# Kernel tuning notes

Hardware: AMD Instinct MI355X
Metric: run time of the kernel (lower is better)

## Reference

```python
import jax, jax.numpy as jnp
import numpy as np

BS, D, NC, N, C, K = 8192, 1024, 64, 100000, 1000, 50


def setup_inputs() -> dict:
    key = jax.random.key(0)
    k1, k2, k3, k4, k5 = jax.random.split(key, 5)
    return {
        "train_embedding": jax.random.normal(k1, (BS, D), dtype=jnp.float32),
        # concept initialized uniform in [-0.5, 0.5] as in init_concept
        "concept": jax.random.uniform(k2, (D, NC), dtype=jnp.float32, minval=-0.5, maxval=0.5),
        "bank": jax.random.normal(k3, (N, D), dtype=jnp.float32),
        "W_h": jax.random.normal(k4, (D, C), dtype=jnp.float32) * 0.02,
        "b_h": jax.random.normal(k5, (C,), dtype=jnp.float32) * 0.02,
        "topk": K,
    }


def reference(train_embedding, concept, bank, W_h, b_h, topk):
    # h_x: linear classifier head
    def h_x(z):
        return z @ W_h + b_h

    # projection onto concept subspace: C (C^T C)^{-1} C^T
    G = concept.T @ concept                      # [nc, nc]
    proj_matrix = concept @ jnp.linalg.inv(G) @ concept.T  # [D, D]
    proj = train_embedding @ proj_matrix.T       # (proj_matrix @ X^T)^T -> [bs, D]
    y_pred = h_x(proj)                           # [bs, C]
    orig_pred = h_x(train_embedding)             # [bs, C]

    # batched per-concept Euclidean distance to the whole bank: [nc, N]
    bank_sq = jnp.sum(bank * bank, axis=1)       # [N]
    con_sq = jnp.sum(concept * concept, axis=0)  # [nc]
    d2 = con_sq[:, None] - 2.0 * (concept.T @ bank.T) + bank_sq[None, :]
    dist = jnp.sqrt(jnp.maximum(d2, 0.0))
    # topk SMALLEST distances per concept
    _, idx = jax.lax.top_k(-dist, topk)          # idx: [nc, k]
    knn = bank[idx]                              # [nc, k, D] gather

    # L_sparse_1: mean over concepts of (c . mean_k knn)
    dots = jnp.einsum('dn,nkd->n', concept, knn) / topk  # [nc]
    L_sparse_1 = jnp.mean(dots)

    nc = concept.shape[1]
    eye = jnp.eye(nc, dtype=concept.dtype)
    L_sparse_2 = jnp.mean(G * (1.0 - eye))       # off-diagonal mean
    norm_metrics = jnp.mean(G * eye)             # diagonal mean

    return (orig_pred, y_pred, L_sparse_1, L_sparse_2, norm_metrics)
```

## Files before the change

kernel.cpp:

```cpp
#include <hip/hip_runtime.h>
#include <cstddef>

#define BSZ   8192
#define DIM   1024
#define NCON  64
#define NBANK 100000
#define NCLS  1000
#define TOPK  50
#define NCHUNK 32
#define CHUNK  3125
#define CHUNKP 3328
#define NDIST 1563

#define Y_OFF 8192000
#define S_OFF 16384000

typedef __attribute__((ext_vector_type(8))) short bf16x8;
typedef __attribute__((ext_vector_type(4))) float f32x4;

__device__ __forceinline__ short f2bf(float x) {
    unsigned u = __builtin_bit_cast(unsigned, x);
    unsigned r = (u + 0x7fffu + ((u >> 16) & 1u)) >> 16;
    return (short)r;
}

__device__ __forceinline__ bf16x8 pack8(f32x4 a, f32x4 b) {
    bf16x8 p;
    p[0] = f2bf(a[0]); p[1] = f2bf(a[1]); p[2] = f2bf(a[2]); p[3] = f2bf(a[3]);
    p[4] = f2bf(b[0]); p[5] = f2bf(b[1]); p[6] = f2bf(b[2]); p[7] = f2bf(b[3]);
    return p;
}

__device__ __forceinline__ void gload16(const void* g, void* l) {
    __builtin_amdgcn_global_load_lds(
        (__attribute__((address_space(1))) void*)g,
        (__attribute__((address_space(3))) void*)l,
        16, 0, 0);
}

__global__ void __launch_bounds__(256) prep_kernel(const float* __restrict__ cpt,
                                                   const float* __restrict__ Wh,
                                                   short* __restrict__ WhT,
                                                   short* __restrict__ cptT) {
    __shared__ short Ts[64][65];
    int b = blockIdx.x;
    int t = threadIdx.x;
    if (b < 256) {
        int k0 = (b & 15) * 64, n0 = (b >> 4) * 64;
        #pragma unroll
        for (int i = 0; i < 16; ++i) {
            int u = i * 256 + t;
            int kL = u >> 6, nL = u & 63;
            int n = n0 + nL;
            Ts[kL][nL] = (n < NCLS) ? f2bf(Wh[(size_t)(k0 + kL) * NCLS + n]) : (short)0;
        }
        __syncthreads();
        #pragma unroll
        for (int i = 0; i < 16; ++i) {
            int u = i * 256 + t;
            int nL = u >> 6, kL = u & 63;
            WhT[(size_t)(n0 + nL) * DIM + k0 + kL] = Ts[kL][nL];
        }
    } else {
        int q = b - 256;
        #pragma unroll
        for (int i = 0; i < 16; ++i) {
            int u = q * 4096 + i * 256 + t;
            int d = u >> 6, n = u & 63;
            cptT[n * DIM + d] = f2bf(cpt[u]);
        }
    }
}

__global__ void __launch_bounds__(256) mid_kernel(const float* __restrict__ bank,
                                                  const float* __restrict__ X,
                                                  const short* __restrict__ cptT,
                                                  const short* __restrict__ WhT,
                                                  short* __restrict__ Xbf,
                                                  short* __restrict__ XCbf,
                                                  float* __restrict__ key,
                                                  float* __restrict__ bank_sq,
                                                  short* __restrict__ MbfT,
                                                  float* __restrict__ G,
                                                  short* __restrict__ invGbf) {
    __shared__ __align__(16) char smem[49152];
    int b = blockIdx.x;
    int t = threadIdx.x;
    int wid = t >> 6, l = t & 63, lr = l & 15, lg = l >> 4;
    if (b < 8) {
        int c0 = b * 128;
        f32x4 acc[4][2] = {};
        for (int kk = 0; kk < DIM; kk += 32) {
            bf16x8 af[4], bfr[2];
            #pragma unroll
            for (int mi = 0; mi < 4; ++mi)
                af[mi] = *(const bf16x8*)(cptT + (mi * 16 + lr) * DIM + kk + lg * 8);
            #pragma unroll
            for (int ni = 0; ni < 2; ++ni)
                bfr[ni] = *(const bf16x8*)(WhT + (size_t)(c0 + wid * 32 + ni * 16 + lr) * DIM + kk + lg * 8);
            #pragma unroll
            for (int mi = 0; mi < 4; ++mi)
                #pragma unroll
                for (int ni = 0; ni < 2; ++ni)
                    acc[mi][ni] = __builtin_amdgcn_mfma_f32_16x16x32_bf16(af[mi], bfr[ni], acc[mi][ni], 0, 0, 0);
        }
        #pragma unroll
        for (int mi = 0; mi < 4; ++mi)
            #pragma unroll
            for (int ni = 0; ni < 2; ++ni)
                #pragma unroll
                for (int r = 0; r < 4; ++r) {
                    int m = mi * 16 + lg * 4 + r;
                    int c = c0 + wid * 32 + ni * 16 + lr;
                    MbfT[(size_t)c * NCON + m] = f2bf(acc[mi][ni][r]);
                }
    } else if (b == 8) {
        float* rowk = (float*)smem;
        float* fk = (float*)(smem + 256);
        f32x4 acc[4] = {};
        for (int kk = 0; kk < DIM; kk += 32) {
            bf16x8 af[4], bfr;
            #pragma unroll
            for (int mi = 0; mi < 4; ++mi)
                af[mi] = *(const bf16x8*)(cptT + (mi * 16 + lr) * DIM + kk + lg * 8);
            bfr = *(const bf16x8*)(cptT + (wid * 16 + lr) * DIM + kk + lg * 8);
            #pragma unroll
            for (int mi = 0; mi < 4; ++mi)
                acc[mi] = __builtin_amdgcn_mfma_f32_16x16x32_bf16(af[mi], bfr, acc[mi], 0, 0, 0);
        }
        #pragma unroll
        for (int mi = 0; mi < 4; ++mi)
            #pragma unroll
            for (int r = 0; r < 4; ++r)
                G[(mi * 16 + lg * 4 + r) * 64 + wid * 16 + lr] = acc[mi][r];
        __syncthreads();
        float myA[16];
        #pragma unroll
        for (int s = 0; s < 16; ++s) myA[s] = G[(4 * s + wid) * 64 + l];
        #pragma unroll
        for (int k = 0; k < 64; ++k) {
            if (wid == (k & 3)) rowk[l] = myA[k >> 2];
            if (l == k) {
                #pragma unroll
                for (int s = 0; s < 16; ++s) fk[4 * s + wid] = myA[s];
            }
            __syncthreads();
            float ip = 1.f / rowk[k];
            float rv = rowk[l];
            #pragma unroll
            for (int s = 0; s < 16; ++s) {
                int i = 4 * s + wid;
                float fv = fk[i];
                float nv;
                if (i == k && l == k)      nv = ip;
                else if (i == k)           nv = rv * ip;
                else if (l == k)           nv = -fv * ip;
                else                       nv = myA[s] - fv * (rv * ip);
                myA[s] = nv;
            }
            __syncthreads();
        }
        #pragma unroll
        for (int s = 0; s < 16; ++s) invGbf[(4 * s + wid) * 64 + l] = f2bf(myA[s]);
    } else if (b < 73) {
        int r0 = (b - 9) * 128;
        int r_[2];
        const float* xrow[2];
        #pragma unroll
        for (int ni = 0; ni < 2; ++ni) {
            r_[ni] = r0 + wid * 32 + ni * 16 + lr;
            xrow[ni] = X + (size_t)r_[ni] * DIM + lg * 8;
        }
        f32x4 acc[4][2] = {};
        for (int kk = 0; kk < DIM; kk += 32) {
            bf16x8 af[4];
            #pragma unroll
            for (int mi = 0; mi < 4; ++mi)
                af[mi] = *(const bf16x8*)(cptT + (mi * 16 + lr) * DIM + kk + lg * 8);
            #pragma unroll
            for (int ni = 0; ni < 2; ++ni) {
                f32x4 a = *(const f32x4*)(xrow[ni] + kk);
                f32x4 c = *(const f32x4*)(xrow[ni] + kk + 4);
                bf16x8 pk = pack8(a, c);
                *(bf16x8*)(Xbf + (size_t)r_[ni] * DIM + kk + lg * 8) = pk;
                #pragma unroll
                for (int mi = 0; mi < 4; ++mi)
                    acc[mi][ni] = __builtin_amdgcn_mfma_f32_16x16x32_bf16(af[mi], pk, acc[mi][ni], 0, 0, 0);
            }
        }
        #pragma unroll
        for (int mi = 0; mi < 4; ++mi)
            #pragma unroll
            for (int ni = 0; ni < 2; ++ni)
                #pragma unroll
                for (int r = 0; r < 4; ++r) {
                    int m = mi * 16 + lg * 4 + r;
                    XCbf[(size_t)r_[ni] * NCON + m] = f2bf(acc[mi][ni][r]);
                }
    } else {
        int j0 = (b - 73) * 64;
        int bj4[4], bs4[4];
        #pragma unroll
        for (int i = 0; i < 4; ++i) {
            int flat = i * 4096 + wid * 1024 + l * 16;
            bj4[i] = flat >> 8;
            bs4[i] = ((flat >> 4) & 15) ^ (bj4[i] & 15);
        }
        int cm2[2], cs2[2];
        #pragma unroll
        for (int i = 0; i < 2; ++i) {
            int flat = i * 4096 + wid * 1024 + l * 16;
            cm2[i] = flat >> 7;
            cs2[i] = ((flat >> 4) & 7) ^ (cm2[i] & 7);
        }
        int jl = wid * 16 + lr;
        f32x4 acc[4] = {};
        float sq = 0.f;
        #pragma unroll
        for (int i = 0; i < 4; ++i) {
            int jr = j0 + bj4[i]; if (jr >= NBANK) jr = NBANK - 1;
            gload16(bank + (size_t)jr * DIM + bs4[i] * 4, smem + i * 4096 + wid * 1024);
        }
        #pragma unroll
        for (int i = 0; i < 2; ++i)
            gload16(cptT + cm2[i] * DIM + cs2[i] * 8, smem + 32768 + i * 4096 + wid * 1024);
        int buf = 0;
        for (int kk = 0; kk < DIM; kk += 64) {
            __syncthreads();
            int kn = kk + 64;
            int nb = buf ^ 1;
            if (kn < DIM) {
                #pragma unroll
                for (int i = 0; i < 4; ++i) {
                    int jr = j0 + bj4[i]; if (jr >= NBANK) jr = NBANK - 1;
                    gload16(bank + (size_t)jr * DIM + kn + bs4[i] * 4,
                            smem + nb * 16384 + i * 4096 + wid * 1024);
                }
                #pragma unroll
                for (int i = 0; i < 2; ++i)
                    gload16(cptT + cm2[i] * DIM + kn + cs2[i] * 8,
                            smem + 32768 + nb * 8192 + i * 4096 + wid * 1024);
            }
            const float* bT = (const float*)(smem + buf * 16384);
            const short* cS = (const short*)(smem + 32768 + buf * 8192);
            #pragma unroll
            for (int ks = 0; ks < 2; ++ks) {
                bf16x8 af[4];
                #pragma unroll
                for (int mi = 0; mi < 4; ++mi) {
                    int m = mi * 16 + lr;
                    af[mi] = *(const bf16x8*)(cS + m * 64 + (((ks * 4 + lg) ^ (m & 7)) << 3));
                }
                int g0 = ks * 8 + lg * 2;
                f32x4 a = *(const f32x4*)(bT + jl * 64 + ((g0 ^ (jl & 15)) << 2));
                f32x4 c = *(const f32x4*)(bT + jl * 64 + (((g0 + 1) ^ (jl & 15)) << 2));
                sq += a[0]*a[0] + a[1]*a[1] + a[2]*a[2] + a[3]*a[3]
                    + c[0]*c[0] + c[1]*c[1] + c[2]*c[2] + c[3]*c[3];
                bf16x8 pk = pack8(a, c);
                #pragma unroll
                for (int mi = 0; mi < 4; ++mi)
                    acc[mi] = __builtin_amdgcn_mfma_f32_16x16x32_bf16(af[mi], pk, acc[mi], 0, 0, 0);
            }
            buf ^= 1;
        }
        sq += __shfl_xor(sq, 16);
        sq += __shfl_xor(sq, 32);
        int j = j0 + jl;
        if (j < NBANK) {
            if (lg == 0) bank_sq[j] = sq;
            #pragma unroll
            for (int mi = 0; mi < 4; ++mi)
                #pragma unroll
                for (int r = 0; r < 4; ++r) {
                    int m = mi * 16 + lg * 4 + r;
                    key[(size_t)m * NBANK + j] = sq - 2.f * acc[mi][r];
                }
        }
    }
}

__global__ void __launch_bounds__(256) topA_kernel(const float* __restrict__ key,
                                                   float* __restrict__ cand_v,
                                                   int* __restrict__ cand_j,
                                                   const short* __restrict__ invGbf,
                                                   const short* __restrict__ MbfT,
                                                   short* __restrict__ M2T) {
    __shared__ float vals[CHUNKP];
    __shared__ float wv[4];
    __shared__ int wj[4];
    int b = blockIdx.x;
    int t = threadIdx.x;
    if (b < 2048) {
        int n = b >> 5;
        int c = b & 31;
        int base = c * CHUNK;
        const float* row = key + (size_t)n * NBANK + base;
        float lv = __builtin_inff();
        int lj = 0x7fffffff;
        #pragma unroll 13
        for (int i = 0; i < 13; ++i) {
            int j = t + i * 256;
            float v = (j < CHUNK) ? row[j] : __builtin_inff();
            vals[j] = v;
            if (v < lv) { lv = v; lj = j; }
        }
        __syncthreads();
        float* cv = cand_v + (size_t)b * TOPK;
        int* cj = cand_j + (size_t)b * TOPK;
        for (int it = 0; it < TOPK; ++it) {
            float bv = lv; int bj = lj;
            #pragma unroll
            for (int o = 32; o > 0; o >>= 1) {
                float ov = __shfl_down(bv, o);
                int oj = __shfl_down(bj, o);
                if (ov < bv || (ov == bv && oj < bj)) { bv = ov; bj = oj; }
            }
            if ((t & 63) == 0) { wv[t >> 6] = bv; wj[t >> 6] = bj; }
            __syncthreads();
            float gv = wv[0]; int gj = wj[0];
            #pragma unroll
            for (int w2 = 1; w2 < 4; ++w2)
                if (wv[w2] < gv || (wv[w2] == gv && wj[w2] < gj)) { gv = wv[w2]; gj = wj[w2]; }
            if (t == 0) { cv[it] = gv; cj[it] = base + gj; }
            if (t == (gj & 255)) {
                vals[gj] = __builtin_inff();
                lv = __builtin_inff(); lj = 0x7fffffff;
                #pragma unroll 13
                for (int i = 0; i < 13; ++i) {
                    int j = t + i * 256;
                    float v = vals[j];
                    if (v < lv) { lv = v; lj = j; }
                }
            }
            __syncthreads();
        }
    } else {
        int c0 = (b - 2048) * 128;
        int wid = t >> 6, l = t & 63, lr = l & 15, lg = l >> 4;
        f32x4 acc[4][2] = {};
        #pragma unroll
        for (int ks = 0; ks < 2; ++ks) {
            bf16x8 af[4], bfr[2];
            #pragma unroll
            for (int mi = 0; mi < 4; ++mi)
                af[mi] = *(const bf16x8*)(invGbf + (mi * 16 + lr) * NCON + ks * 32 + lg * 8);
            #pragma unroll
            for (int ni = 0; ni < 2; ++ni)
                bfr[ni] = *(const bf16x8*)(MbfT + (size_t)(c0 + wid * 32 + ni * 16 + lr) * NCON + ks * 32 + lg * 8);
            #pragma unroll
            for (int mi = 0; mi < 4; ++mi)
                #pragma unroll
                for (int ni = 0; ni < 2; ++ni)
                    acc[mi][ni] = __builtin_amdgcn_mfma_f32_16x16x32_bf16(af[mi], bfr[ni], acc[mi][ni], 0, 0, 0);
        }
        #pragma unroll
        for (int mi = 0; mi < 4; ++mi)
            #pragma unroll
            for (int ni = 0; ni < 2; ++ni)
                #pragma unroll
                for (int r = 0; r < 4; ++r) {
                    int n = mi * 16 + lg * 4 + r;
                    int c = c0 + wid * 32 + ni * 16 + lr;
                    M2T[(size_t)c * NCON + n] = f2bf(acc[mi][ni][r]);
                }
    }
}

__global__ void __launch_bounds__(256) pred_kernel(const short* __restrict__ Xbf,
                                                   const short* __restrict__ WhT,
                                                   const short* __restrict__ XCbf,
                                                   const short* __restrict__ M2T,
                                                   const float* __restrict__ bh,
                                                   const float* __restrict__ cand_v,
                                                   const int* __restrict__ cand_j,
                                                   const float* __restrict__ bank_sq,
                                                   float* __restrict__ orig,
                                                   float* __restrict__ ypred,
                                                   float* __restrict__ dots) {
    __shared__ __align__(16) char smem[32768];
    int b = blockIdx.x;
    int t = threadIdx.x;
    int wid = t >> 6, l = t & 63, lr = l & 15, lg = l >> 4;
    if (b < 512) {
        short* As = (short*)smem;
        short* Bs = (short*)(smem + 16384);
        int c0 = (b & 7) * 128;
        int r0 = (b >> 3) * 128;
        int wr = wid >> 1, wc = wid & 1;
        int srow_off = l >> 3;
        int scol = ((l & 7) ^ (l >> 3)) * 8;
        f32x4 acc[4][4] = {};
        for (int kk = 0; kk < DIM; kk += 64) {
            if (kk) __syncthreads();
            #pragma unroll
            for (int i = 0; i < 4; ++i) {
                int si = wid * 4 + i;
                int row = si * 8 + srow_off;
                gload16(Xbf + (size_t)(r0 + row) * DIM + kk + scol, As + si * 512);
                gload16(WhT + (size_t)(c0 + row) * DIM + kk + scol, Bs + si * 512);
            }
            __syncthreads();
            #pragma unroll
            for (int ks = 0; ks < 2; ++ks) {
                bf16x8 af[4], bfr[4];
                #pragma unroll
                for (int mi = 0; mi < 4; ++mi) {
                    int rr = wr * 64 + mi * 16 + lr;
                    int slot = (ks * 4 + lg) ^ (rr & 7);
                    af[mi] = *(const bf16x8*)(As + rr * 64 + slot * 8);
                }
                #pragma unroll
                for (int ni = 0; ni < 4; ++ni) {
                    int cc = wc * 64 + ni * 16 + lr;
                    int slot = (ks * 4 + lg) ^ (cc & 7);
                    bfr[ni] = *(const bf16x8*)(Bs + cc * 64 + slot * 8);
                }
                #pragma unroll
                for (int mi = 0; mi < 4; ++mi)
                    #pragma unroll
                    for (int ni = 0; ni < 4; ++ni)
                        acc[mi][ni] = __builtin_amdgcn_mfma_f32_16x16x32_bf16(af[mi], bfr[ni], acc[mi][ni], 0, 0, 0);
            }
        }
        #pragma unroll
        for (int mi = 0; mi < 4; ++mi)
            #pragma unroll
            for (int ni = 0; ni < 4; ++ni) {
                int col = c0 + wc * 64 + ni * 16 + lr;
                if (col < NCLS) {
                    float bias = bh[col];
                    #pragma unroll
                    for (int r = 0; r < 4; ++r) {
                        int row = r0 + wr * 64 + mi * 16 + lg * 4 + r;
                        orig[(size_t)row * NCLS + col] = acc[mi][ni][r] + bias;
                    }
                }
            }
    } else if (b < 1024) {
        int q = b - 512;
        int c0 = (q & 7) * 128;
        int r0 = (q >> 3) * 128;
        int wr = wid >> 1, wc = wid & 1;
        f32x4 acc[4][4] = {};
        #pragma unroll
        for (int ks = 0; ks < 2; ++ks) {
            bf16x8 af[4], bfr[4];
            #pragma unroll
            for (int mi = 0; mi < 4; ++mi)
                af[mi] = *(const bf16x8*)(XCbf + (size_t)(r0 + wr * 64 + mi * 16 + lr) * NCON + ks * 32 + lg * 8);
            #pragma unroll
            for (int ni = 0; ni < 4; ++ni)
                bfr[ni] = *(const bf16x8*)(M2T + (size_t)(c0 + wc * 64 + ni * 16 + lr) * NCON + ks * 32 + lg * 8);
            #pragma unroll
            for (int mi = 0; mi < 4; ++mi)
                #pragma unroll
                for (int ni = 0; ni < 4; ++ni)
                    acc[mi][ni] = __builtin_amdgcn_mfma_f32_16x16x32_bf16(af[mi], bfr[ni], acc[mi][ni], 0, 0, 0);
        }
        #pragma unroll
        for (int mi = 0; mi < 4; ++mi)
            #pragma unroll
            for (int ni = 0; ni < 4; ++ni) {
                int col = c0 + wc * 64 + ni * 16 + lr;
                if (col < NCLS) {
                    float bias = bh[col];
                    #pragma unroll
                    for (int r = 0; r < 4; ++r) {
                        int row = r0 + wr * 64 + mi * 16 + lg * 4 + r;
                        ypred[(size_t)row * NCLS + col] = acc[mi][ni][r] + bias;
                    }
                }
            }
    } else {
        int n = b - 1024;
        const int NC2 = NCHUNK * TOPK;
        float* vals = (float*)smem;
        int* gidx = (int*)(smem + 6400);
        float* wv = (float*)(smem + 12800);
        int* wj = (int*)(smem + 12816);
        int* wl = (int*)(smem + 12832);
        for (int j = t; j < NC2; j += 256) {
            vals[j] = cand_v[(size_t)n * NC2 + j];
            gidx[j] = cand_j[(size_t)n * NC2 + j];
        }
        __syncthreads();
        float sum = 0.f;
        for (int it = 0; it < TOPK; ++it) {
            float bv = __builtin_inff();
            int bj = 0x7fffffff;
            int bl = -1;
            #pragma unroll 7
            for (int j = t; j < NC2; j += 256) {
                float v = vals[j];
                int gj = gidx[j];
                if (v < bv || (v == bv && gj < bj)) { bv = v; bj = gj; bl = j; }
            }
            #pragma unroll
            for (int o = 32; o > 0; o >>= 1) {
                float ov = __shfl_down(bv, o);
                int oj = __shfl_down(bj, o);
                int ol = __shfl_down(bl, o);
                if (ov < bv || (ov == bv && oj < bj)) { bv = ov; bj = oj; bl = ol; }
            }
            if ((t & 63) == 0) { wv[t >> 6] = bv; wj[t >> 6] = bj; wl[t >> 6] = bl; }
            __syncthreads();
            if (t == 0) {
                #pragma unroll
                for (int w2 = 1; w2 < 4; ++w2)
                    if (wv[w2] < bv || (wv[w2] == bv && wj[w2] < bj)) { bv = wv[w2]; bj = wj[w2]; bl = wl[w2]; }
                sum += 0.5f * (bank_sq[bj] - bv);
                vals[bl] = __builtin_inff();
            }
            __syncthreads();
        }
        if (t == 0) dots[n] = sum / (float)TOPK;
    }
}

__global__ void __launch_bounds__(256) fin_kernel(const float* __restrict__ G,
                                                  const float* __restrict__ dots,
                                                  float* __restrict__ out3) {
    __shared__ float r1[256], r2[256], r3[256];
    int t = threadIdx.x;
    float sd = 0.f, so = 0.f;
    for (int u = t; u < 4096; u += 256) {
        float g = G[u];
        if ((u >> 6) == (u & 63)) sd += g; else so += g;
    }
    float s1 = (t < NCON) ? dots[t] : 0.f;
    r1[t] = sd; r2[t] = so; r3[t] = s1;
    __syncthreads();
    for (int o = 128; o > 0; o >>= 1) {
        if (t < o) { r1[t] += r1[t + o]; r2[t] += r2[t + o]; r3[t] += r3[t + o]; }
        __syncthreads();
    }
    if (t == 0) {
        out3[0] = r3[0] / 64.f;
        out3[1] = r2[0] / 4096.f;
        out3[2] = r1[0] / 4096.f;
    }
}

extern "C" void kernel_launch(void* const* d_in, const int* in_sizes, int n_in,
                              void* d_out, int out_size, void* d_ws, size_t ws_size,
                              hipStream_t stream) {
    const float* X    = (const float*)d_in[0];
    const float* cpt  = (const float*)d_in[1];
    const float* bank = (const float*)d_in[2];
    const float* Wh   = (const float*)d_in[3];
    const float* bh   = (const float*)d_in[4];
    float* out = (float*)d_out;

    float* orig  = out;
    float* ypred = out + Y_OFF;
    float* out3  = out + S_OFF;

    char* w = (char*)d_ws;
    short* Xbf    = (short*)(w);
    short* WhT    = (short*)(w + 16777216);
    short* cptT   = (short*)(w + 18874368);
    short* XCbf   = (short*)(w + 19005440);
    short* M2T    = (short*)(w + 20054016);
    float* key    = (float*)(w + 20185088);
    float* bank_sq= (float*)(w + 45785088);
    float* G      = (float*)(w + 46185472);
    short* invGbf = (short*)(w + 46201856);
    short* MbfT   = (short*)(w + 46210048);
    float* cand_v = (float*)(w + 46341120);
    int*   cand_j = (int*)  (w + 46750720);
    float* dots   = (float*)(w + 47160320);

    prep_kernel<<<272, 256, 0, stream>>>(cpt, Wh, WhT, cptT);
    mid_kernel<<<73 + NDIST, 256, 0, stream>>>(bank, X, cptT, WhT, Xbf, XCbf, key, bank_sq, MbfT, G, invGbf);
    topA_kernel<<<2056, 256, 0, stream>>>(key, cand_v, cand_j, invGbf, MbfT, M2T);
    pred_kernel<<<1088, 256, 0, stream>>>(Xbf, WhT, XCbf, M2T, bh, cand_v, cand_j, bank_sq, orig, ypred, dots);
    fin_kernel<<<1, 256, 0, stream>>>(G, dots, out3);
}
```

Before: 378.9 us.

## Rebalance kernel stages: split distance GEMM, co-schedule aux work with top-k

Moves the bank-distance GEMM into its own kernel. The small auxiliary GEMMs (X projections, M, G and the inverse) now run in the same launch as the first top-k stage, the M2 product moves into the pred kernel, and the ypred GEMM is fused with the final reduction. The intent is to overlap the cheap auxiliary work with the memory-bound top-k scan and to shorten the dependency chains between launches. The risk is the shared-memory footprint of the merged kernels and a tail imbalance from mixing heterogeneous block types in one launch.

New measurement: 413.1 us. +9.0%, slower.

```diff
diff --git a/kernel.cpp b/kernel.cpp
--- a/kernel.cpp
+++ b/kernel.cpp
@@ -72,18 +72,108 @@
     }
 }
 
-__global__ void __launch_bounds__(256) mid_kernel(const float* __restrict__ bank,
-                                                  const float* __restrict__ X,
-                                                  const short* __restrict__ cptT,
-                                                  const short* __restrict__ WhT,
-                                                  short* __restrict__ Xbf,
-                                                  short* __restrict__ XCbf,
-                                                  float* __restrict__ key,
-                                                  float* __restrict__ bank_sq,
-                                                  short* __restrict__ MbfT,
-                                                  float* __restrict__ G,
-                                                  short* __restrict__ invGbf) {
+__global__ void __launch_bounds__(256) dist_kernel(const float* __restrict__ bank,
+                                                   const short* __restrict__ cptT,
+                                                   float* __restrict__ key,
+                                                   float* __restrict__ bank_sq) {
     __shared__ __align__(16) char smem[49152];
+    int b = blockIdx.x;
+    int t = threadIdx.x;
+    int wid = t >> 6, l = t & 63, lr = l & 15, lg = l >> 4;
+    int j0 = b * 64;
+    int bj4[4], bs4[4];
+    #pragma unroll
+    for (int i = 0; i < 4; ++i) {
+        int flat = i * 4096 + wid * 1024 + l * 16;
+        bj4[i] = flat >> 8;
+        bs4[i] = ((flat >> 4) & 15) ^ (bj4[i] & 15);
+    }
+    int cm2[2], cs2[2];
+    #pragma unroll
+    for (int i = 0; i < 2; ++i) {
+        int flat = i * 4096 + wid * 1024 + l * 16;
+        cm2[i] = flat >> 7;
+        cs2[i] = ((flat >> 4) & 7) ^ (cm2[i] & 7);
+    }
+    int jl = wid * 16 + lr;
+    f32x4 acc[4] = {};
+    float sq = 0.f;
+    #pragma unroll
+    for (int i = 0; i < 4; ++i) {
+        int jr = j0 + bj4[i]; if (jr >= NBANK) jr = NBANK - 1;
+        gload16(bank + (size_t)jr * DIM + bs4[i] * 4, smem + i * 4096 + wid * 1024);
+    }
+    #pragma unroll
+    for (int i = 0; i < 2; ++i)
+        gload16(cptT + cm2[i] * DIM + cs2[i] * 8, smem + 32768 + i * 4096 + wid * 1024);
+    int buf = 0;
+    for (int kk = 0; kk < DIM; kk += 64) {
+        __syncthreads();
+        int kn = kk + 64;
+        int nb = buf ^ 1;
+        if (kn < DIM) {
+            #pragma unroll
+            for (int i = 0; i < 4; ++i) {
+                int jr = j0 + bj4[i]; if (jr >= NBANK) jr = NBANK - 1;
+                gload16(bank + (size_t)jr * DIM + kn + bs4[i] * 4,
+                        smem + nb * 16384 + i * 4096 + wid * 1024);
+            }
+            #pragma unroll
+            for (int i = 0; i < 2; ++i)
+                gload16(cptT + cm2[i] * DIM + kn + cs2[i] * 8,
+                        smem + 32768 + nb * 8192 + i * 4096 + wid * 1024);
+        }
+        const float* bT = (const float*)(smem + buf * 16384);
+        const short* cS = (const short*)(smem + 32768 + buf * 8192);
+        #pragma unroll
+        for (int ks = 0; ks < 2; ++ks) {
+            bf16x8 af[4];
+            #pragma unroll
+            for (int mi = 0; mi < 4; ++mi) {
+                int m = mi * 16 + lr;
+                af[mi] = *(const bf16x8*)(cS + m * 64 + (((ks * 4 + lg) ^ (m & 7)) << 3));
+            }
+            int g0 = ks * 8 + lg * 2;
+            f32x4 a = *(const f32x4*)(bT + jl * 64 + ((g0 ^ (jl & 15)) << 2));
+            f32x4 c = *(const f32x4*)(bT + jl * 64 + (((g0 + 1) ^ (jl & 15)) << 2));
+            sq += a[0]*a[0] + a[1]*a[1] + a[2]*a[2] + a[3]*a[3]
+                + c[0]*c[0] + c[1]*c[1] + c[2]*c[2] + c[3]*c[3];
+            bf16x8 pk = pack8(a, c);
+            #pragma unroll
+            for (int mi = 0; mi < 4; ++mi)
+                acc[mi] = __builtin_amdgcn_mfma_f32_16x16x32_bf16(af[mi], pk, acc[mi], 0, 0, 0);
+        }
+        buf ^= 1;
+    }
+    sq += __shfl_xor(sq, 16);
+    sq += __shfl_xor(sq, 32);
+    int j = j0 + jl;
+    if (j < NBANK) {
+        if (lg == 0) bank_sq[j] = sq;
+        #pragma unroll
+        for (int mi = 0; mi < 4; ++mi)
+            #pragma unroll
+            for (int r = 0; r < 4; ++r) {
+                int m = mi * 16 + lg * 4 + r;
+                key[(size_t)m * NBANK + j] = sq - 2.f * acc[mi][r];
+            }
+    }
+}
+
+__global__ void __launch_bounds__(256) aux_topA_kernel(const float* __restrict__ X,
+                                                       const short* __restrict__ cptT,
+                                                       const short* __restrict__ WhT,
+                                                       const float* __restrict__ key,
+                                                       short* __restrict__ Xbf,
+                                                       short* __restrict__ XCbf,
+                                                       short* __restrict__ MbfT,
+                                                       float* __restrict__ G,
+                                                       short* __restrict__ invGbf,
+                                                       float* __restrict__ cand_v,
+                                                       int* __restrict__ cand_j) {
+    __shared__ float vals[CHUNKP];
+    __shared__ float wv[4];
+    __shared__ int wj[4];
     int b = blockIdx.x;
     int t = threadIdx.x;
     int wid = t >> 6, l = t & 63, lr = l & 15, lg = l >> 4;
@@ -115,8 +205,8 @@
                     MbfT[(size_t)c * NCON + m] = f2bf(acc[mi][ni][r]);
                 }
     } else if (b == 8) {
-        float* rowk = (float*)smem;
-        float* fk = (float*)(smem + 256);
+        float* rowk = vals;
+        float* fk = vals + 64;
         f32x4 acc[4] = {};
         for (int kk = 0; kk < DIM; kk += 32) {
             bf16x8 af[4], bfr;
@@ -198,101 +288,9 @@
                     XCbf[(size_t)r_[ni] * NCON + m] = f2bf(acc[mi][ni][r]);
                 }
     } else {
-        int j0 = (b - 73) * 64;
-        int bj4[4], bs4[4];
-        #pragma unroll
-        for (int i = 0; i < 4; ++i) {
-            int flat = i * 4096 + wid * 1024 + l * 16;
-            bj4[i] = flat >> 8;
-            bs4[i] = ((flat >> 4) & 15) ^ (bj4[i] & 15);
-        }
-        int cm2[2], cs2[2];
-        #pragma unroll
-        for (int i = 0; i < 2; ++i) {
-            int flat = i * 4096 + wid * 1024 + l * 16;
-            cm2[i] = flat >> 7;
-            cs2[i] = ((flat >> 4) & 7) ^ (cm2[i] & 7);
-        }
-        int jl = wid * 16 + lr;
-        f32x4 acc[4] = {};
-        float sq = 0.f;
-        #pragma unroll
-        for (int i = 0; i < 4; ++i) {
-            int jr = j0 + bj4[i]; if (jr >= NBANK) jr = NBANK - 1;
-            gload16(bank + (size_t)jr * DIM + bs4[i] * 4, smem + i * 4096 + wid * 1024);
-        }
-        #pragma unroll
-        for (int i = 0; i < 2; ++i)
-            gload16(cptT + cm2[i] * DIM + cs2[i] * 8, smem + 32768 + i * 4096 + wid * 1024);
-        int buf = 0;
-        for (int kk = 0; kk < DIM; kk += 64) {
-            __syncthreads();
-            int kn = kk + 64;
-            int nb = buf ^ 1;
-            if (kn < DIM) {
-                #pragma unroll
-                for (int i = 0; i < 4; ++i) {
-                    int jr = j0 + bj4[i]; if (jr >= NBANK) jr = NBANK - 1;
-                    gload16(bank + (size_t)jr * DIM + kn + bs4[i] * 4,
-                            smem + nb * 16384 + i * 4096 + wid * 1024);
-                }
-                #pragma unroll
-                for (int i = 0; i < 2; ++i)
-                    gload16(cptT + cm2[i] * DIM + kn + cs2[i] * 8,
-                            smem + 32768 + nb * 8192 + i * 4096 + wid * 1024);
-            }
-            const float* bT = (const float*)(smem + buf * 16384);
-            const short* cS = (const short*)(smem + 32768 + buf * 8192);
-            #pragma unroll
-            for (int ks = 0; ks < 2; ++ks) {
-                bf16x8 af[4];
-                #pragma unroll
-                for (int mi = 0; mi < 4; ++mi) {
-                    int m = mi * 16 + lr;
-                    af[mi] = *(const bf16x8*)(cS + m * 64 + (((ks * 4 + lg) ^ (m & 7)) << 3));
-                }
-                int g0 = ks * 8 + lg * 2;
-                f32x4 a = *(const f32x4*)(bT + jl * 64 + ((g0 ^ (jl & 15)) << 2));
-                f32x4 c = *(const f32x4*)(bT + jl * 64 + (((g0 + 1) ^ (jl & 15)) << 2));
-                sq += a[0]*a[0] + a[1]*a[1] + a[2]*a[2] + a[3]*a[3]
-                    + c[0]*c[0] + c[1]*c[1] + c[2]*c[2] + c[3]*c[3];
-                bf16x8 pk = pack8(a, c);
-                #pragma unroll
-                for (int mi = 0; mi < 4; ++mi)
-                    acc[mi] = __builtin_amdgcn_mfma_f32_16x16x32_bf16(af[mi], pk, acc[mi], 0, 0, 0);
-            }
-            buf ^= 1;
-        }
-        sq += __shfl_xor(sq, 16);
-        sq += __shfl_xor(sq, 32);
-        int j = j0 + jl;
-        if (j < NBANK) {
-            if (lg == 0) bank_sq[j] = sq;
-            #pragma unroll
-            for (int mi = 0; mi < 4; ++mi)
-                #pragma unroll
-                for (int r = 0; r < 4; ++r) {
-                    int m = mi * 16 + lg * 4 + r;
-                    key[(size_t)m * NBANK + j] = sq - 2.f * acc[mi][r];
-                }
-        }
-    }
-}
-
-__global__ void __launch_bounds__(256) topA_kernel(const float* __restrict__ key,
-                                                   float* __restrict__ cand_v,
-                                                   int* __restrict__ cand_j,
-                                                   const short* __restrict__ invGbf,
-                                                   const short* __restrict__ MbfT,
-                                                   short* __restrict__ M2T) {
-    __shared__ float vals[CHUNKP];
-    __shared__ float wv[4];
-    __shared__ int wj[4];
-    int b = blockIdx.x;
-    int t = threadIdx.x;
-    if (b < 2048) {
-        int n = b >> 5;
-        int c = b & 31;
+        int q = b - 73;
+        int n = q >> 5;
+        int c = q & 31;
         int base = c * CHUNK;
         const float* row = key + (size_t)n * NBANK + base;
         float lv = __builtin_inff();
@@ -305,8 +303,8 @@
             if (v < lv) { lv = v; lj = j; }
         }
         __syncthreads();
-        float* cv = cand_v + (size_t)b * TOPK;
-        int* cj = cand_j + (size_t)b * TOPK;
+        float* cv = cand_v + (size_t)q * TOPK;
+        int* cj = cand_j + (size_t)q * TOPK;
         for (int it = 0; it < TOPK; ++it) {
             float bv = lv; int bj = lj;
             #pragma unroll
@@ -334,48 +332,19 @@
             }
             __syncthreads();
         }
-    } else {
-        int c0 = (b - 2048) * 128;
-        int wid = t >> 6, l = t & 63, lr = l & 15, lg = l >> 4;
-        f32x4 acc[4][2] = {};
-        #pragma unroll
-        for (int ks = 0; ks < 2; ++ks) {
-            bf16x8 af[4], bfr[2];
-            #pragma unroll
-            for (int mi = 0; mi < 4; ++mi)
-                af[mi] = *(const bf16x8*)(invGbf + (mi * 16 + lr) * NCON + ks * 32 + lg * 8);
-            #pragma unroll
-            for (int ni = 0; ni < 2; ++ni)
-                bfr[ni] = *(const bf16x8*)(MbfT + (size_t)(c0 + wid * 32 + ni * 16 + lr) * NCON + ks * 32 + lg * 8);
-            #pragma unroll
-            for (int mi = 0; mi < 4; ++mi)
-                #pragma unroll
-                for (int ni = 0; ni < 2; ++ni)
-                    acc[mi][ni] = __builtin_amdgcn_mfma_f32_16x16x32_bf16(af[mi], bfr[ni], acc[mi][ni], 0, 0, 0);
-        }
-        #pragma unroll
-        for (int mi = 0; mi < 4; ++mi)
-            #pragma unroll
-            for (int ni = 0; ni < 2; ++ni)
-                #pragma unroll
-                for (int r = 0; r < 4; ++r) {
-                    int n = mi * 16 + lg * 4 + r;
-                    int c = c0 + wid * 32 + ni * 16 + lr;
-                    M2T[(size_t)c * NCON + n] = f2bf(acc[mi][ni][r]);
-                }
     }
 }
 
 __global__ void __launch_bounds__(256) pred_kernel(const short* __restrict__ Xbf,
                                                    const short* __restrict__ WhT,
-                                                   const short* __restrict__ XCbf,
-                                                   const short* __restrict__ M2T,
+                                                   const short* __restrict__ invGbf,
+                                                   const short* __restrict__ MbfT,
                                                    const float* __restrict__ bh,
                                                    const float* __restrict__ cand_v,
                                                    const int* __restrict__ cand_j,
                                                    const float* __restrict__ bank_sq,
                                                    float* __restrict__ orig,
-                                                   float* __restrict__ ypred,
+                                                   short* __restrict__ M2T,
                                                    float* __restrict__ dots) {
     __shared__ __align__(16) char smem[32768];
     int b = blockIdx.x;
@@ -436,43 +405,36 @@
                     }
                 }
             }
-    } else if (b < 1024) {
-        int q = b - 512;
-        int c0 = (q & 7) * 128;
-        int r0 = (q >> 3) * 128;
-        int wr = wid >> 1, wc = wid & 1;
-        f32x4 acc[4][4] = {};
+    } else if (b < 520) {
+        int c0 = (b - 512) * 128;
+        f32x4 acc[4][2] = {};
         #pragma unroll
         for (int ks = 0; ks < 2; ++ks) {
-            bf16x8 af[4], bfr[4];
-            #pragma unroll
-            for (int mi = 0; mi < 4; ++mi)
-                af[mi] = *(const bf16x8*)(XCbf + (size_t)(r0 + wr * 64 + mi * 16 + lr) * NCON + ks * 32 + lg * 8);
-            #pragma unroll
-            for (int ni = 0; ni < 4; ++ni)
-                bfr[ni] = *(const bf16x8*)(M2T + (size_t)(c0 + wc * 64 + ni * 16 + lr) * NCON + ks * 32 + lg * 8);
-            #pragma unroll
-            for (int mi = 0; mi < 4; ++mi)
-                #pragma unroll
-                for (int ni = 0; ni < 4; ++ni)
+            bf16x8 af[4], bfr[2];
+            #pragma unroll
+            for (int mi = 0; mi < 4; ++mi)
+                af[mi] = *(const bf16x8*)(invGbf + (mi * 16 + lr) * NCON + ks * 32 + lg * 8);
+            #pragma unroll
+            for (int ni = 0; ni < 2; ++ni)
+                bfr[ni] = *(const bf16x8*)(MbfT + (size_t)(c0 + wid * 32 + ni * 16 + lr) * NCON + ks * 32 + lg * 8);
+            #pragma unroll
+            for (int mi = 0; mi < 4; ++mi)
+                #pragma unroll
+                for (int ni = 0; ni < 2; ++ni)
                     acc[mi][ni] = __builtin_amdgcn_mfma_f32_16x16x32_bf16(af[mi], bfr[ni], acc[mi][ni], 0, 0, 0);
         }
         #pragma unroll
         for (int mi = 0; mi < 4; ++mi)
             #pragma unroll
-            for (int ni = 0; ni < 4; ++ni) {
-                int col = c0 + wc * 64 + ni * 16 + lr;
-                if (col < NCLS) {
-                    float bias = bh[col];
-                    #pragma unroll
-                    for (int r = 0; r < 4; ++r) {
-                        int row = r0 + wr * 64 + mi * 16 + lg * 4 + r;
-                        ypred[(size_t)row * NCLS + col] = acc[mi][ni][r] + bias;
-                    }
-                }
-            }
+            for (int ni = 0; ni < 2; ++ni)
+                #pragma unroll
+                for (int r = 0; r < 4; ++r) {
+                    int n = mi * 16 + lg * 4 + r;
+                    int c = c0 + wid * 32 + ni * 16 + lr;
+                    M2T[(size_t)c * NCON + n] = f2bf(acc[mi][ni][r]);
+                }
     } else {
-        int n = b - 1024;
+        int n = b - 520;
         const int NC2 = NCHUNK * TOPK;
         float* vals = (float*)smem;
         int* gidx = (int*)(smem + 6400);
@@ -517,27 +479,69 @@
     }
 }
 
-__global__ void __launch_bounds__(256) fin_kernel(const float* __restrict__ G,
-                                                  const float* __restrict__ dots,
-                                                  float* __restrict__ out3) {
+__global__ void __launch_bounds__(256) ypred_fin_kernel(const short* __restrict__ XCbf,
+                                                        const short* __restrict__ M2T,
+                                                        const float* __restrict__ bh,
+                                                        const float* __restrict__ G,
+                                                        const float* __restrict__ dots,
+                                                        float* __restrict__ ypred,
+                                                        float* __restrict__ out3) {
     __shared__ float r1[256], r2[256], r3[256];
+    int b = blockIdx.x;
     int t = threadIdx.x;
-    float sd = 0.f, so = 0.f;
-    for (int u = t; u < 4096; u += 256) {
-        float g = G[u];
-        if ((u >> 6) == (u & 63)) sd += g; else so += g;
-    }
-    float s1 = (t < NCON) ? dots[t] : 0.f;
-    r1[t] = sd; r2[t] = so; r3[t] = s1;
-    __syncthreads();
-    for (int o = 128; o > 0; o >>= 1) {
-        if (t < o) { r1[t] += r1[t + o]; r2[t] += r2[t + o]; r3[t] += r3[t + o]; }
+    if (b < 512) {
+        int wid = t >> 6, l = t & 63, lr = l & 15, lg = l >> 4;
+        int c0 = (b & 7) * 128;
+        int r0 = (b >> 3) * 128;
+        int wr = wid >> 1, wc = wid & 1;
+        f32x4 acc[4][4] = {};
+        #pragma unroll
+        for (int ks = 0; ks < 2; ++ks) {
+            bf16x8 af[4], bfr[4];
+            #pragma unroll
+            for (int mi = 0; mi < 4; ++mi)
+                af[mi] = *(const bf16x8*)(XCbf + (size_t)(r0 + wr * 64 + mi * 16 + lr) * NCON + ks * 32 + lg * 8);
+            #pragma unroll
+            for (int ni = 0; ni < 4; ++ni)
+                bfr[ni] = *(const bf16x8*)(M2T + (size_t)(c0 + wc * 64 + ni * 16 + lr) * NCON + ks * 32 + lg * 8);
+            #pragma unroll
+            for (int mi = 0; mi < 4; ++mi)
+                #pragma unroll
+                for (int ni = 0; ni < 4; ++ni)
+                    acc[mi][ni] = __builtin_amdgcn_mfma_f32_16x16x32_bf16(af[mi], bfr[ni], acc[mi][ni], 0, 0, 0);
+        }
+        #pragma unroll
+        for (int mi = 0; mi < 4; ++mi)
+            #pragma unroll
+            for (int ni = 0; ni < 4; ++ni) {
+                int col = c0 + wc * 64 + ni * 16 + lr;
+                if (col < NCLS) {
+                    float bias = bh[col];
+                    #pragma unroll
+                    for (int r = 0; r < 4; ++r) {
+                        int row = r0 + wr * 64 + mi * 16 + lg * 4 + r;
+                        ypred[(size_t)row * NCLS + col] = acc[mi][ni][r] + bias;
+                    }
+                }
+            }
+    } else {
+        float sd = 0.f, so = 0.f;
+        for (int u = t; u < 4096; u += 256) {
+            float g = G[u];
+            if ((u >> 6) == (u & 63)) sd += g; else so += g;
+        }
+        float s1 = (t < NCON) ? dots[t] : 0.f;
+        r1[t] = sd; r2[t] = so; r3[t] = s1;
         __syncthreads();
-    }
-    if (t == 0) {
-        out3[0] = r3[0] / 64.f;
-        out3[1] = r2[0] / 4096.f;
-        out3[2] = r1[0] / 4096.f;
+        for (int o = 128; o > 0; o >>= 1) {
+            if (t < o) { r1[t] += r1[t + o]; r2[t] += r2[t + o]; r3[t] += r3[t + o]; }
+            __syncthreads();
+        }
+        if (t == 0) {
+            out3[0] = r3[0] / 64.f;
+            out3[1] = r2[0] / 4096.f;
+            out3[2] = r1[0] / 4096.f;
+        }
     }
 }
 
@@ -571,8 +575,8 @@
     float* dots   = (float*)(w + 47160320);
 
     prep_kernel<<<272, 256, 0, stream>>>(cpt, Wh, WhT, cptT);
-    mid_kernel<<<73 + NDIST, 256, 0, stream>>>(bank, X, cptT, WhT, Xbf, XCbf, key, bank_sq, MbfT, G, invGbf);
-    topA_kernel<<<2056, 256, 0, stream>>>(key, cand_v, cand_j, invGbf, MbfT, M2T);
-    pred_kernel<<<1088, 256, 0, stream>>>(Xbf, WhT, XCbf, M2T, bh, cand_v, cand_j, bank_sq, orig, ypred, dots);
-    fin_kernel<<<1, 256, 0, stream>>>(G, dots, out3);
-}
+    dist_kernel<<<NDIST, 256, 0, stream>>>(bank, cptT, key, bank_sq);
+    aux_topA_kernel<<<73 + 2048, 256, 0, stream>>>(X, cptT, WhT, key, Xbf, XCbf, MbfT, G, invGbf, cand_v, cand_j);
+    pred_kernel<<<584, 256, 0, stream>>>(Xbf, WhT, invGbf, MbfT, bh, cand_v, cand_j, bank_sq, orig, M2T, dots);
+    ypred_fin_kernel<<<513, 256, 0, stream>>>(XCbf, M2T, bh, G, dots, ypred, out3);
+}
```
